# Kernel optimization log

Hardware: AMD Instinct MI355X
Metric: run time of the kernel (lower is better)

## Reference

```python
import jax, jax.numpy as jnp
import numpy as np

N, D_MODEL, D_FFN, K = 8192, 1024, 4096, 512


def setup_inputs() -> dict:
    key = jax.random.key(0)
    ks = jax.random.split(key, 5)
    x = jax.random.normal(ks[0], (N, D_MODEL), dtype=jnp.float32)
    topk_indices = jax.random.randint(ks[1], (N, K), 0, D_FFN, dtype=jnp.int32)
    scale = 0.02
    w_gate = jax.random.normal(ks[2], (D_MODEL, D_FFN), dtype=jnp.float32) * scale
    w_up = jax.random.normal(ks[3], (D_MODEL, D_FFN), dtype=jnp.float32) * scale
    w_down = jax.random.normal(ks[4], (D_FFN, D_MODEL), dtype=jnp.float32) * scale
    return {"x": x, "topk_indices": topk_indices, "w_gate": w_gate, "w_up": w_up, "w_down": w_down}


def reference(x, topk_indices, w_gate, w_up, w_down):
    # Dense gate/up projections: [N, d_ffn]
    G = x @ w_gate
    U = x @ w_up
    # Gather only the top-k active neurons per token and fuse SwiGLU there.
    G_act = jnp.take_along_axis(G, topk_indices, axis=1)  # [N, k]
    U_act = jnp.take_along_axis(U, topk_indices, axis=1)  # [N, k]
    Z_active = jax.nn.silu(G_act) * U_act                 # [N, k]
    # Sparse-to-dense down projection: scatter active activations back into
    # the d_ffn axis (zeros elsewhere), then dense matmul with w_down.
    n, k = topk_indices.shape
    rows = jnp.arange(n, dtype=topk_indices.dtype)[:, None]
    Z_dense = jnp.zeros((n, w_down.shape[0]), dtype=Z_active.dtype).at[rows, topk_indices].add(Z_active)
    return Z_dense @ w_down  # [N, d_model]
```

## Files before the change

### kernel.cpp

```cpp
#include <hip/hip_runtime.h>
#include <hip/hip_bf16.h>
#include <cstdint>
#include <cstddef>

#define N_TOK   8192
#define D_MODEL 1024
#define D_FFN   4096
#define K_TOP   512
#define NHALF   2048

typedef __bf16 bf16_t;
typedef __bf16 bf16x8 __attribute__((ext_vector_type(8)));
typedef __bf16 bf16x4 __attribute__((ext_vector_type(4)));
typedef float  f32x4  __attribute__((ext_vector_type(4)));


__global__ void cvt_f32_bf16(const float* __restrict__ in, bf16_t* __restrict__ out, int n4) {
  int i = blockIdx.x * blockDim.x + threadIdx.x;
  if (i < n4) {
    const f32x4 v = ((const f32x4*)in)[i];
    bf16x4 o;
    o[0] = (bf16_t)v[0]; o[1] = (bf16_t)v[1]; o[2] = (bf16_t)v[2]; o[3] = (bf16_t)v[3];
    ((bf16x4*)out)[i] = o;
  }
}

__global__ void transpose_cvt(const float* __restrict__ in, bf16_t* __restrict__ out,
                              int rows, int cols) {
  __shared__ float tile[32][33];
  const int tx = threadIdx.x, ty = threadIdx.y;
  const int x = blockIdx.x * 32 + tx;
#pragma unroll
  for (int i = 0; i < 32; i += 8) {
    int y = blockIdx.y * 32 + ty + i;
    tile[ty + i][tx] = in[(size_t)y * cols + x];
  }
  __syncthreads();
  const int xo = blockIdx.y * 32 + tx;
#pragma unroll
  for (int i = 0; i < 32; i += 8) {
    int yo = blockIdx.x * 32 + ty + i;
    out[(size_t)yo * rows + xo] = (bf16_t)tile[tx][ty + i];
  }
}

#define ROWS_PER_BLK 4
__global__ __launch_bounds__(256) void count_scatter_lds(
    const int* __restrict__ idx, unsigned int* __restrict__ M) {
  __shared__ unsigned int loc[ROWS_PER_BLK * (D_FFN / 8)];
  const int t = threadIdx.x;
  const int r0 = blockIdx.x * ROWS_PER_BLK;

#pragma unroll
  for (int i = 0; i < ROWS_PER_BLK * (D_FFN / 8) / 256; ++i)
    loc[t + i * 256] = 0;
  __syncthreads();

  const int* ip = idx + (size_t)r0 * K_TOP;
#pragma unroll
  for (int i = 0; i < ROWS_PER_BLK * K_TOP / 256; ++i) {
    const int e = t + i * 256;
    const int lr = e >> 9;
    const int j = ip[e];
    atomicAdd(&loc[lr * (D_FFN / 8) + (j >> 3)], 1u << ((j & 7) * 4));
  }
  __syncthreads();

  unsigned int* op = M + (size_t)r0 * (D_FFN / 8);
#pragma unroll
  for (int i = 0; i < ROWS_PER_BLK * (D_FFN / 8) / 256; ++i)
    op[t + i * 256] = loc[t + i * 256];
}


__device__ __forceinline__ void gload_lds16(const void* g, void* l) {
#if __has_builtin(__builtin_amdgcn_global_load_lds)
  __builtin_amdgcn_global_load_lds((__attribute__((address_space(1))) void*)(g),
                                   (__attribute__((address_space(3))) void*)(l), 16, 0, 0);
#else
  *(bf16x8*)l = *(const bf16x8*)g;
#endif
}

#define MFMA16(ACC, AF, BF)                                                      \
  _Pragma("unroll")                                                              \
  for (int m = 0; m < 4; ++m)                                                    \
    _Pragma("unroll")                                                            \
    for (int n = 0; n < 4; ++n)                                                  \
      ACC[m][n] = __builtin_amdgcn_mfma_f32_16x16x32_bf16(AF[m], BF[n], ACC[m][n], 0, 0, 0);

#define BM1 256
#define BN1 128
#define BK1 64
#define NT1 (D_MODEL / BK1)
#define LDSBUF 65536

__global__ __launch_bounds__(512, 2) void gemm_gateup_2p(
    const bf16_t* __restrict__ A,
    const bf16_t* __restrict__ Bg,
    const bf16_t* __restrict__ Bu,
    const unsigned int* __restrict__ cnt,
    bf16_t* __restrict__ Z,
    int n_base)
{
  extern __shared__ char smem[];
  const int t = threadIdx.x;
  const int lane = t & 63;
  const int w = t >> 6;
  const int wr = w >> 1;
  const int wc = w & 1;
  const int l15 = lane & 15;
  const int grp = lane >> 4;
  const int m0 = blockIdx.x * BM1;
  const int n0 = blockIdx.y * BN1;

  int offA[4], offB[2];
#pragma unroll
  for (int c = 0; c < 4; ++c) {
    const int s = c * 512 + w * 64 + lane;
    const int r = s >> 3, cb = (s & 7) ^ (r & 7);
    offA[c] = (m0 + r) * D_MODEL + cb * 8;
  }
#pragma unroll
  for (int c = 0; c < 2; ++c) {
    const int s = c * 512 + w * 64 + lane;
    const int r = s >> 3, cb = (s & 7) ^ (r & 7);
    offB[c] = (n_base + n0 + r) * D_MODEL + cb * 8;
  }
  const int dst0 = (w * 64 + lane) * 16;

  const int swz = l15 & 7;
  const int a_k0 = wr * 8192 + l15 * 128 + ((0 + grp) ^ swz) * 16;
  const int a_k1 = wr * 8192 + l15 * 128 + ((4 + grp) ^ swz) * 16;
  const int bg_k0 = 32768 + wc * 8192 + l15 * 128 + ((0 + grp) ^ swz) * 16;
  const int bg_k1 = 32768 + wc * 8192 + l15 * 128 + ((4 + grp) ^ swz) * 16;
  const int bu_k0 = bg_k0 + 16384;
  const int bu_k1 = bg_k1 + 16384;

#pragma unroll
  for (int c = 0; c < 4; ++c) gload_lds16(A + offA[c], smem + dst0 + c * 8192);
#pragma unroll
  for (int c = 0; c < 2; ++c) gload_lds16(Bg + offB[c], smem + 32768 + dst0 + c * 8192);
#pragma unroll
  for (int c = 0; c < 2; ++c) gload_lds16(Bu + offB[c], smem + 49152 + dst0 + c * 8192);
  asm volatile("s_waitcnt vmcnt(0)" ::: "memory");
  __builtin_amdgcn_s_barrier();

  f32x4 accg[4][4] = {};
  f32x4 accu[4][4] = {};

  for (int tt = 0; tt < NT1; ++tt) {
    char* rb = smem + (tt & 1) * LDSBUF;
    char* wb = smem + ((tt & 1) ^ 1) * LDSBUF;
    const int kg = (tt + 1) * BK1;
    const bool st = (tt + 1 < NT1);
    bf16x8 af0[4], af1[4], bg0[4], bg1[4], bu0[4], bu1[4];

#pragma unroll
    for (int m = 0; m < 4; ++m) {
      af0[m] = *(const bf16x8*)(rb + a_k0 + m * 2048);
      af1[m] = *(const bf16x8*)(rb + a_k1 + m * 2048);
    }
#pragma unroll
    for (int n = 0; n < 4; ++n) {
      bg0[n] = *(const bf16x8*)(rb + bg_k0 + n * 2048);
      bg1[n] = *(const bf16x8*)(rb + bg_k1 + n * 2048);
    }
    if (st) {
#pragma unroll
      for (int c = 0; c < 4; ++c) gload_lds16(A + offA[c] + kg, wb + dst0 + c * 8192);
#pragma unroll
      for (int c = 0; c < 2; ++c) gload_lds16(Bg + offB[c] + kg, wb + 32768 + dst0 + c * 8192);
#pragma unroll
      for (int c = 0; c < 2; ++c) gload_lds16(Bu + offB[c] + kg, wb + 49152 + dst0 + c * 8192);
    }
    __builtin_amdgcn_s_barrier();
    asm volatile("s_waitcnt lgkmcnt(0)" ::: "memory");
    __builtin_amdgcn_s_setprio(1);
    MFMA16(accg, af0, bg0);
    MFMA16(accg, af1, bg1);
    __builtin_amdgcn_s_setprio(0);
    __builtin_amdgcn_s_barrier();

#pragma unroll
    for (int n = 0; n < 4; ++n) {
      bu0[n] = *(const bf16x8*)(rb + bu_k0 + n * 2048);
      bu1[n] = *(const bf16x8*)(rb + bu_k1 + n * 2048);
    }
    asm volatile("s_waitcnt lgkmcnt(0)" ::: "memory");
    __builtin_amdgcn_s_setprio(1);
    MFMA16(accu, af0, bu0);
    MFMA16(accu, af1, bu1);
    __builtin_amdgcn_s_setprio(0);
    if (st) asm volatile("s_waitcnt vmcnt(0)" ::: "memory");
    __builtin_amdgcn_s_barrier();
  }

#pragma unroll
  for (int m = 0; m < 4; ++m) {
#pragma unroll
    for (int n = 0; n < 4; ++n) {
      const int colL = n0 + wc * 64 + n * 16 + l15;
      const int jg = n_base + colL;
#pragma unroll
      for (int j = 0; j < 4; ++j) {
        const int row = m0 + wr * 64 + m * 16 + grp * 4 + j;
        float g = accg[m][n][j];
        float u = accu[m][n][j];
        unsigned int cw = cnt[(size_t)row * (D_FFN / 8) + (jg >> 3)];
        float c = (float)((cw >> ((jg & 7) * 4)) & 15u);
        float z = c * u * (g / (1.0f + __expf(-g)));
        Z[(size_t)row * NHALF + colL] = (bf16_t)z;
      }
    }
  }
}

#define BM2 256
#define BN2 128
#define BK2 64
#define NT2 (NHALF / BK2)
#define LDSBUF2 49152

__global__ __launch_bounds__(512, 2) void gemm_down_1p(
    const bf16_t* __restrict__ A,
    const bf16_t* __restrict__ B,
    float* __restrict__ C,
    int k_base, int accum)
{
  extern __shared__ char smem[];
  const int t = threadIdx.x;
  const int lane = t & 63;
  const int w = t >> 6;
  const int wr = w >> 1;
  const int wc = w & 1;
  const int l15 = lane & 15;
  const int grp = lane >> 4;
  const int m0 = blockIdx.x * BM2;
  const int n0 = blockIdx.y * BN2;

  int offA[4], offB[2];
#pragma unroll
  for (int c = 0; c < 4; ++c) {
    const int s = c * 512 + w * 64 + lane;
    const int r = s >> 3, cb = (s & 7) ^ (r & 7);
    offA[c] = (m0 + r) * NHALF + cb * 8;
  }
#pragma unroll
  for (int c = 0; c < 2; ++c) {
    const int s = c * 512 + w * 64 + lane;
    const int r = s >> 3, cb = (s & 7) ^ (r & 7);
    offB[c] = (n0 + r) * D_FFN + k_base + cb * 8;
  }
  const int dst0 = (w * 64 + lane) * 16;

  const int swz = l15 & 7;
  const int a_k0 = wr * 8192 + l15 * 128 + ((0 + grp) ^ swz) * 16;
  const int a_k1 = wr * 8192 + l15 * 128 + ((4 + grp) ^ swz) * 16;
  const int b_k0 = 32768 + wc * 8192 + l15 * 128 + ((0 + grp) ^ swz) * 16;
  const int b_k1 = 32768 + wc * 8192 + l15 * 128 + ((4 + grp) ^ swz) * 16;

#pragma unroll
  for (int c = 0; c < 4; ++c) gload_lds16(A + offA[c], smem + dst0 + c * 8192);
#pragma unroll
  for (int c = 0; c < 2; ++c) gload_lds16(B + offB[c], smem + 32768 + dst0 + c * 8192);
  asm volatile("s_waitcnt vmcnt(0)" ::: "memory");
  __builtin_amdgcn_s_barrier();

  f32x4 acc[4][4] = {};

  for (int tt = 0; tt < NT2; ++tt) {
    char* rb = smem + (tt & 1) * LDSBUF2;
    char* wb = smem + ((tt & 1) ^ 1) * LDSBUF2;
    const int kg = (tt + 1) * BK2;
    const bool st = (tt + 1 < NT2);
    bf16x8 af0[4], af1[4], bf0[4], bf1[4];

#pragma unroll
    for (int m = 0; m < 4; ++m) {
      af0[m] = *(const bf16x8*)(rb + a_k0 + m * 2048);
      af1[m] = *(const bf16x8*)(rb + a_k1 + m * 2048);
    }
#pragma unroll
    for (int n = 0; n < 4; ++n) {
      bf0[n] = *(const bf16x8*)(rb + b_k0 + n * 2048);
      bf1[n] = *(const bf16x8*)(rb + b_k1 + n * 2048);
    }
    if (st) {
#pragma unroll
      for (int c = 0; c < 4; ++c) gload_lds16(A + offA[c] + kg, wb + dst0 + c * 8192);
#pragma unroll
      for (int c = 0; c < 2; ++c) gload_lds16(B + offB[c] + kg, wb + 32768 + dst0 + c * 8192);
    }
    __builtin_amdgcn_s_barrier();
    asm volatile("s_waitcnt lgkmcnt(0)" ::: "memory");
    __builtin_amdgcn_s_setprio(1);
    MFMA16(acc, af0, bf0);
    MFMA16(acc, af1, bf1);
    __builtin_amdgcn_s_setprio(0);
    if (st) asm volatile("s_waitcnt vmcnt(0)" ::: "memory");
    __builtin_amdgcn_s_barrier();
  }

#pragma unroll
  for (int m = 0; m < 4; ++m) {
#pragma unroll
    for (int n = 0; n < 4; ++n) {
      const int col = n0 + wc * 64 + n * 16 + l15;
#pragma unroll
      for (int j = 0; j < 4; ++j) {
        const int row = m0 + wr * 64 + m * 16 + grp * 4 + j;
        const size_t off = (size_t)row * D_MODEL + col;
        float prev = accum ? C[off] : 0.0f;
        C[off] = prev + acc[m][n][j];
      }
    }
  }
}


extern "C" void kernel_launch(void* const* d_in, const int* in_sizes, int n_in,
                              void* d_out, int out_size, void* d_ws, size_t ws_size,
                              hipStream_t stream) {
  const float* x  = (const float*)d_in[0];
  const int*   idx = (const int*)d_in[1];
  const float* wg = (const float*)d_in[2];
  const float* wu = (const float*)d_in[3];
  const float* wd = (const float*)d_in[4];
  float* out = (float*)d_out;

  char* ws = (char*)d_ws;
  const size_t SZ_XB  = (size_t)N_TOK * D_MODEL * 2;
  const size_t SZ_W   = (size_t)D_MODEL * D_FFN * 2;
  const size_t SZ_CNT = (size_t)N_TOK * D_FFN / 2;
  bf16_t* xb  = (bf16_t*)(ws);
  bf16_t* wgT = (bf16_t*)(ws + SZ_XB);
  bf16_t* wuT = (bf16_t*)(ws + SZ_XB + SZ_W);
  bf16_t* wdT = (bf16_t*)(ws + SZ_XB + 2 * SZ_W);
  unsigned int* cnt = (unsigned int*)(ws + SZ_XB + 3 * SZ_W);
  bf16_t* Z   = (bf16_t*)(ws + SZ_XB + 3 * SZ_W + SZ_CNT);

  (void)hipFuncSetAttribute((const void*)gemm_gateup_2p,
                            hipFuncAttributeMaxDynamicSharedMemorySize, 131072);
  (void)hipFuncSetAttribute((const void*)gemm_down_1p,
                            hipFuncAttributeMaxDynamicSharedMemorySize, 98304);

  count_scatter_lds<<<N_TOK / ROWS_PER_BLK, 256, 0, stream>>>(idx, cnt);
  cvt_f32_bf16<<<(N_TOK * D_MODEL / 4 + 255) / 256, 256, 0, stream>>>(x, xb, N_TOK * D_MODEL / 4);
  transpose_cvt<<<dim3(D_FFN / 32, D_MODEL / 32), dim3(32, 8), 0, stream>>>(wg, wgT, D_MODEL, D_FFN);
  transpose_cvt<<<dim3(D_FFN / 32, D_MODEL / 32), dim3(32, 8), 0, stream>>>(wu, wuT, D_MODEL, D_FFN);
  transpose_cvt<<<dim3(D_MODEL / 32, D_FFN / 32), dim3(32, 8), 0, stream>>>(wd, wdT, D_FFN, D_MODEL);

  gemm_gateup_2p<<<dim3(N_TOK / BM1, NHALF / BN1), 512, 131072, stream>>>(xb, wgT, wuT, cnt, Z, 0);
  gemm_down_1p<<<dim3(N_TOK / BM2, D_MODEL / BN2), 512, 98304, stream>>>(Z, wdT, out, 0, 0);
  gemm_gateup_2p<<<dim3(N_TOK / BM1, NHALF / BN1), 512, 131072, stream>>>(xb, wgT, wuT, cnt, Z, NHALF);
  gemm_down_1p<<<dim3(N_TOK / BM2, D_MODEL / BN2), 512, 98304, stream>>>(Z, wdT, out, NHALF, 1);
}
```

Baseline: 266.5 us.

## Switch gate/up and down GEMMs to triple-buffered BK=32 pipelines with register prefetch

Both GEMM kernels move from double-buffered BK=64 tiles to triple-buffered BK=32 tiles. Global-to-LDS loads are issued two stages ahead, and the next tile's LDS fragments are prefetched into registers during the MFMAs, which leaves one barrier per iteration instead of two. LDS use drops to 96KB and 72KB, and the down kernel's launch bounds ask for 4 blocks per CU. The goal is to hide memory latency and cut barrier stalls, at the cost of more iterations, tighter vmcnt bookkeeping and possible register pressure.

```diff
diff --git a/kernel.cpp b/kernel.cpp
--- a/kernel.cpp
+++ b/kernel.cpp
@@ -89,13 +89,14 @@
     for (int n = 0; n < 4; ++n)                                                  \
       ACC[m][n] = __builtin_amdgcn_mfma_f32_16x16x32_bf16(AF[m], BF[n], ACC[m][n], 0, 0, 0);
 
+
 #define BM1 256
 #define BN1 128
-#define BK1 64
+#define BK1 32
 #define NT1 (D_MODEL / BK1)
-#define LDSBUF 65536
-
-__global__ __launch_bounds__(512, 2) void gemm_gateup_2p(
+#define GU_BUF 32768
+
+__global__ __launch_bounds__(512, 2) void gemm_gateup_3b(
     const bf16_t* __restrict__ A,
     const bf16_t* __restrict__ Bg,
     const bf16_t* __restrict__ Bu,
@@ -114,86 +115,72 @@
   const int m0 = blockIdx.x * BM1;
   const int n0 = blockIdx.y * BN1;
 
-  int offA[4], offB[2];
-#pragma unroll
-  for (int c = 0; c < 4; ++c) {
-    const int s = c * 512 + w * 64 + lane;
-    const int r = s >> 3, cb = (s & 7) ^ (r & 7);
-    offA[c] = (m0 + r) * D_MODEL + cb * 8;
-  }
-#pragma unroll
-  for (int c = 0; c < 2; ++c) {
-    const int s = c * 512 + w * 64 + lane;
-    const int r = s >> 3, cb = (s & 7) ^ (r & 7);
-    offB[c] = (n_base + n0 + r) * D_MODEL + cb * 8;
-  }
-  const int dst0 = (w * 64 + lane) * 16;
-
-  const int swz = l15 & 7;
-  const int a_k0 = wr * 8192 + l15 * 128 + ((0 + grp) ^ swz) * 16;
-  const int a_k1 = wr * 8192 + l15 * 128 + ((4 + grp) ^ swz) * 16;
-  const int bg_k0 = 32768 + wc * 8192 + l15 * 128 + ((0 + grp) ^ swz) * 16;
-  const int bg_k1 = 32768 + wc * 8192 + l15 * 128 + ((4 + grp) ^ swz) * 16;
-  const int bu_k0 = bg_k0 + 16384;
-  const int bu_k1 = bg_k1 + 16384;
-
-#pragma unroll
-  for (int c = 0; c < 4; ++c) gload_lds16(A + offA[c], smem + dst0 + c * 8192);
-#pragma unroll
-  for (int c = 0; c < 2; ++c) gload_lds16(Bg + offB[c], smem + 32768 + dst0 + c * 8192);
-#pragma unroll
-  for (int c = 0; c < 2; ++c) gload_lds16(Bu + offB[c], smem + 49152 + dst0 + c * 8192);
-  asm volatile("s_waitcnt vmcnt(0)" ::: "memory");
+  const int sA0 = t, sA1 = t + 512;
+  const int rA0 = sA0 >> 2, uA0 = (sA0 & 3) ^ (rA0 & 3);
+  const int rA1 = sA1 >> 2, uA1 = (sA1 & 3) ^ (rA1 & 3);
+  const int rB  = t >> 2,   uB  = (t & 3) ^ (rB & 3);
+  const int gA0 = (m0 + rA0) * D_MODEL + uA0 * 8;
+  const int gA1 = (m0 + rA1) * D_MODEL + uA1 * 8;
+  const int gB  = (n_base + n0 + rB) * D_MODEL + uB * 8;
+  const int dA0 = sA0 * 16, dA1 = sA1 * 16, dB = t * 16;
+
+#define GU_STAGE(ti) do {                                                        \
+    char* _b = smem + ((ti) % 3) * GU_BUF; const int _k = (ti) * BK1;            \
+    gload_lds16(A  + gA0 + _k, _b + dA0);                                        \
+    gload_lds16(A  + gA1 + _k, _b + dA1);                                        \
+    gload_lds16(Bg + gB  + _k, _b + 16384 + dB);                                 \
+    gload_lds16(Bu + gB  + _k, _b + 24576 + dB); } while (0)
+
+  int a_off[4], bg_off[4];
+#pragma unroll
+  for (int m = 0; m < 4; ++m) {
+    const int row = wr * 64 + m * 16 + l15;
+    a_off[m] = row * 64 + ((grp ^ (row & 3)) * 16);
+  }
+#pragma unroll
+  for (int n = 0; n < 4; ++n) {
+    const int row = wc * 64 + n * 16 + l15;
+    bg_off[n] = 16384 + row * 64 + ((grp ^ (row & 3)) * 16);
+  }
+
+  GU_STAGE(0); GU_STAGE(1);
+  asm volatile("s_waitcnt vmcnt(4)" ::: "memory");
   __builtin_amdgcn_s_barrier();
+
+  bf16x8 af[4], bgf[4], buf_[4];
+#pragma unroll
+  for (int m = 0; m < 4; ++m) af[m] = *(const bf16x8*)(smem + a_off[m]);
+#pragma unroll
+  for (int n = 0; n < 4; ++n) bgf[n] = *(const bf16x8*)(smem + bg_off[n]);
 
   f32x4 accg[4][4] = {};
   f32x4 accu[4][4] = {};
 
   for (int tt = 0; tt < NT1; ++tt) {
-    char* rb = smem + (tt & 1) * LDSBUF;
-    char* wb = smem + ((tt & 1) ^ 1) * LDSBUF;
-    const int kg = (tt + 1) * BK1;
-    const bool st = (tt + 1 < NT1);
-    bf16x8 af0[4], af1[4], bg0[4], bg1[4], bu0[4], bu1[4];
-
-#pragma unroll
-    for (int m = 0; m < 4; ++m) {
-      af0[m] = *(const bf16x8*)(rb + a_k0 + m * 2048);
-      af1[m] = *(const bf16x8*)(rb + a_k1 + m * 2048);
-    }
-#pragma unroll
-    for (int n = 0; n < 4; ++n) {
-      bg0[n] = *(const bf16x8*)(rb + bg_k0 + n * 2048);
-      bg1[n] = *(const bf16x8*)(rb + bg_k1 + n * 2048);
-    }
-    if (st) {
-#pragma unroll
-      for (int c = 0; c < 4; ++c) gload_lds16(A + offA[c] + kg, wb + dst0 + c * 8192);
-#pragma unroll
-      for (int c = 0; c < 2; ++c) gload_lds16(Bg + offB[c] + kg, wb + 32768 + dst0 + c * 8192);
-#pragma unroll
-      for (int c = 0; c < 2; ++c) gload_lds16(Bu + offB[c] + kg, wb + 49152 + dst0 + c * 8192);
-    }
+    char* rbuf = smem + (tt % 3) * GU_BUF;
+    if (tt + 2 < NT1) GU_STAGE(tt + 2);
+#pragma unroll
+    for (int n = 0; n < 4; ++n) buf_[n] = *(const bf16x8*)(rbuf + bg_off[n] + 8192);
+    asm volatile("s_waitcnt lgkmcnt(4)" ::: "memory");
+    __builtin_amdgcn_s_setprio(1);
+    MFMA16(accg, af, bgf);
+    __builtin_amdgcn_s_setprio(0);
+    asm volatile("s_waitcnt lgkmcnt(0)" ::: "memory");
+    if (tt + 2 < NT1) { asm volatile("s_waitcnt vmcnt(4)" ::: "memory"); }
+    else              { asm volatile("s_waitcnt vmcnt(0)" ::: "memory"); }
     __builtin_amdgcn_s_barrier();
-    asm volatile("s_waitcnt lgkmcnt(0)" ::: "memory");
+    char* nbuf = smem + ((tt + 1) % 3) * GU_BUF;
+    if (tt + 1 < NT1) {
+#pragma unroll
+      for (int n = 0; n < 4; ++n) bgf[n] = *(const bf16x8*)(nbuf + bg_off[n]);
+    }
     __builtin_amdgcn_s_setprio(1);
-    MFMA16(accg, af0, bg0);
-    MFMA16(accg, af1, bg1);
+    MFMA16(accu, af, buf_);
     __builtin_amdgcn_s_setprio(0);
-    __builtin_amdgcn_s_barrier();
-
-#pragma unroll
-    for (int n = 0; n < 4; ++n) {
-      bu0[n] = *(const bf16x8*)(rb + bu_k0 + n * 2048);
-      bu1[n] = *(const bf16x8*)(rb + bu_k1 + n * 2048);
-    }
-    asm volatile("s_waitcnt lgkmcnt(0)" ::: "memory");
-    __builtin_amdgcn_s_setprio(1);
-    MFMA16(accu, af0, bu0);
-    MFMA16(accu, af1, bu1);
-    __builtin_amdgcn_s_setprio(0);
-    if (st) asm volatile("s_waitcnt vmcnt(0)" ::: "memory");
-    __builtin_amdgcn_s_barrier();
+    if (tt + 1 < NT1) {
+#pragma unroll
+      for (int m = 0; m < 4; ++m) af[m] = *(const bf16x8*)(nbuf + a_off[m]);
+    }
   }
 
 #pragma unroll
@@ -214,16 +201,17 @@
       }
     }
   }
+#undef GU_STAGE
 }
 
 #define BM2 256
 #define BN2 128
-#define BK2 64
+#define BK2 32
 #define NT2 (NHALF / BK2)
-#define LDSBUF2 49152
-
-__global__ __launch_bounds__(512, 2) void gemm_down_1p(
-    const bf16_t* __restrict__ A,
+#define DN_BUF 24576
+
+__global__ __launch_bounds__(512, 4) void gemm_down_3b(
+    const bf16_t* __restrict__ Az,
     const bf16_t* __restrict__ B,
     float* __restrict__ C,
     int k_base, int accum)
@@ -239,67 +227,61 @@
   const int m0 = blockIdx.x * BM2;
   const int n0 = blockIdx.y * BN2;
 
-  int offA[4], offB[2];
-#pragma unroll
-  for (int c = 0; c < 4; ++c) {
-    const int s = c * 512 + w * 64 + lane;
-    const int r = s >> 3, cb = (s & 7) ^ (r & 7);
-    offA[c] = (m0 + r) * NHALF + cb * 8;
-  }
-#pragma unroll
-  for (int c = 0; c < 2; ++c) {
-    const int s = c * 512 + w * 64 + lane;
-    const int r = s >> 3, cb = (s & 7) ^ (r & 7);
-    offB[c] = (n0 + r) * D_FFN + k_base + cb * 8;
-  }
-  const int dst0 = (w * 64 + lane) * 16;
-
-  const int swz = l15 & 7;
-  const int a_k0 = wr * 8192 + l15 * 128 + ((0 + grp) ^ swz) * 16;
-  const int a_k1 = wr * 8192 + l15 * 128 + ((4 + grp) ^ swz) * 16;
-  const int b_k0 = 32768 + wc * 8192 + l15 * 128 + ((0 + grp) ^ swz) * 16;
-  const int b_k1 = 32768 + wc * 8192 + l15 * 128 + ((4 + grp) ^ swz) * 16;
-
-#pragma unroll
-  for (int c = 0; c < 4; ++c) gload_lds16(A + offA[c], smem + dst0 + c * 8192);
-#pragma unroll
-  for (int c = 0; c < 2; ++c) gload_lds16(B + offB[c], smem + 32768 + dst0 + c * 8192);
-  asm volatile("s_waitcnt vmcnt(0)" ::: "memory");
+  const int sA0 = t, sA1 = t + 512;
+  const int rA0 = sA0 >> 2, uA0 = (sA0 & 3) ^ (rA0 & 3);
+  const int rA1 = sA1 >> 2, uA1 = (sA1 & 3) ^ (rA1 & 3);
+  const int rB  = t >> 2,   uB  = (t & 3) ^ (rB & 3);
+  const int gA0 = (m0 + rA0) * NHALF + uA0 * 8;
+  const int gA1 = (m0 + rA1) * NHALF + uA1 * 8;
+  const int gB  = (n0 + rB) * D_FFN + k_base + uB * 8;
+  const int dA0 = sA0 * 16, dA1 = sA1 * 16, dB = t * 16;
+
+#define DN_STAGE(ti) do {                                                        \
+    char* _b = smem + ((ti) % 3) * DN_BUF; const int _k = (ti) * BK2;            \
+    gload_lds16(Az + gA0 + _k, _b + dA0);                                        \
+    gload_lds16(Az + gA1 + _k, _b + dA1);                                        \
+    gload_lds16(B  + gB  + _k, _b + 16384 + dB); } while (0)
+
+  int a_off[4], b_off[4];
+#pragma unroll
+  for (int m = 0; m < 4; ++m) {
+    const int row = wr * 64 + m * 16 + l15;
+    a_off[m] = row * 64 + ((grp ^ (row & 3)) * 16);
+  }
+#pragma unroll
+  for (int n = 0; n < 4; ++n) {
+    const int row = wc * 64 + n * 16 + l15;
+    b_off[n] = 16384 + row * 64 + ((grp ^ (row & 3)) * 16);
+  }
+
+  DN_STAGE(0); DN_STAGE(1);
+  asm volatile("s_waitcnt vmcnt(3)" ::: "memory");
   __builtin_amdgcn_s_barrier();
 
+  bf16x8 af[4], bf[4];
+#pragma unroll
+  for (int m = 0; m < 4; ++m) af[m] = *(const bf16x8*)(smem + a_off[m]);
+#pragma unroll
+  for (int n = 0; n < 4; ++n) bf[n] = *(const bf16x8*)(smem + b_off[n]);
+
   f32x4 acc[4][4] = {};
 
   for (int tt = 0; tt < NT2; ++tt) {
-    char* rb = smem + (tt & 1) * LDSBUF2;
-    char* wb = smem + ((tt & 1) ^ 1) * LDSBUF2;
-    const int kg = (tt + 1) * BK2;
-    const bool st = (tt + 1 < NT2);
-    bf16x8 af0[4], af1[4], bf0[4], bf1[4];
-
-#pragma unroll
-    for (int m = 0; m < 4; ++m) {
-      af0[m] = *(const bf16x8*)(rb + a_k0 + m * 2048);
-      af1[m] = *(const bf16x8*)(rb + a_k1 + m * 2048);
-    }
-#pragma unroll
-    for (int n = 0; n < 4; ++n) {
-      bf0[n] = *(const bf16x8*)(rb + b_k0 + n * 2048);
-      bf1[n] = *(const bf16x8*)(rb + b_k1 + n * 2048);
-    }
-    if (st) {
-#pragma unroll
-      for (int c = 0; c < 4; ++c) gload_lds16(A + offA[c] + kg, wb + dst0 + c * 8192);
-#pragma unroll
-      for (int c = 0; c < 2; ++c) gload_lds16(B + offB[c] + kg, wb + 32768 + dst0 + c * 8192);
-    }
+    if (tt + 2 < NT2) DN_STAGE(tt + 2);
+    __builtin_amdgcn_s_setprio(1);
+    MFMA16(acc, af, bf);
+    __builtin_amdgcn_s_setprio(0);
+    asm volatile("s_waitcnt lgkmcnt(0)" ::: "memory");
+    if (tt + 2 < NT2) { asm volatile("s_waitcnt vmcnt(3)" ::: "memory"); }
+    else              { asm volatile("s_waitcnt vmcnt(0)" ::: "memory"); }
     __builtin_amdgcn_s_barrier();
-    asm volatile("s_waitcnt lgkmcnt(0)" ::: "memory");
-    __builtin_amdgcn_s_setprio(1);
-    MFMA16(acc, af0, bf0);
-    MFMA16(acc, af1, bf1);
-    __builtin_amdgcn_s_setprio(0);
-    if (st) asm volatile("s_waitcnt vmcnt(0)" ::: "memory");
-    __builtin_amdgcn_s_barrier();
+    if (tt + 1 < NT2) {
+      char* nbuf = smem + ((tt + 1) % 3) * DN_BUF;
+#pragma unroll
+      for (int m = 0; m < 4; ++m) af[m] = *(const bf16x8*)(nbuf + a_off[m]);
+#pragma unroll
+      for (int n = 0; n < 4; ++n) bf[n] = *(const bf16x8*)(nbuf + b_off[n]);
+    }
   }
 
 #pragma unroll
@@ -316,6 +298,7 @@
       }
     }
   }
+#undef DN_STAGE
 }
 
 
@@ -340,10 +323,10 @@
   unsigned int* cnt = (unsigned int*)(ws + SZ_XB + 3 * SZ_W);
   bf16_t* Z   = (bf16_t*)(ws + SZ_XB + 3 * SZ_W + SZ_CNT);
 
-  (void)hipFuncSetAttribute((const void*)gemm_gateup_2p,
-                            hipFuncAttributeMaxDynamicSharedMemorySize, 131072);
-  (void)hipFuncSetAttribute((const void*)gemm_down_1p,
-                            hipFuncAttributeMaxDynamicSharedMemorySize, 98304);
+  (void)hipFuncSetAttribute((const void*)gemm_gateup_3b,
+                            hipFuncAttributeMaxDynamicSharedMemorySize, 3 * GU_BUF);
+  (void)hipFuncSetAttribute((const void*)gemm_down_3b,
+                            hipFuncAttributeMaxDynamicSharedMemorySize, 3 * DN_BUF);
 
   count_scatter_lds<<<N_TOK / ROWS_PER_BLK, 256, 0, stream>>>(idx, cnt);
   cvt_f32_bf16<<<(N_TOK * D_MODEL / 4 + 255) / 256, 256, 0, stream>>>(x, xb, N_TOK * D_MODEL / 4);
@@ -351,8 +334,8 @@
   transpose_cvt<<<dim3(D_FFN / 32, D_MODEL / 32), dim3(32, 8), 0, stream>>>(wu, wuT, D_MODEL, D_FFN);
   transpose_cvt<<<dim3(D_MODEL / 32, D_FFN / 32), dim3(32, 8), 0, stream>>>(wd, wdT, D_FFN, D_MODEL);
 
-  gemm_gateup_2p<<<dim3(N_TOK / BM1, NHALF / BN1), 512, 131072, stream>>>(xb, wgT, wuT, cnt, Z, 0);
-  gemm_down_1p<<<dim3(N_TOK / BM2, D_MODEL / BN2), 512, 98304, stream>>>(Z, wdT, out, 0, 0);
-  gemm_gateup_2p<<<dim3(N_TOK / BM1, NHALF / BN1), 512, 131072, stream>>>(xb, wgT, wuT, cnt, Z, NHALF);
-  gemm_down_1p<<<dim3(N_TOK / BM2, D_MODEL / BN2), 512, 98304, stream>>>(Z, wdT, out, NHALF, 1);
-}
+  gemm_gateup_3b<<<dim3(N_TOK / BM1, NHALF / BN1), 512, 3 * GU_BUF, stream>>>(xb, wgT, wuT, cnt, Z, 0);
+  gemm_down_3b<<<dim3(N_TOK / BM2, D_MODEL / BN2), 512, 3 * DN_BUF, stream>>>(Z, wdT, out, 0, 0);
+  gemm_gateup_3b<<<dim3(N_TOK / BM1, NHALF / BN1), 512, 3 * GU_BUF, stream>>>(xb, wgT, wuT, cnt, Z, NHALF);
+  gemm_down_3b<<<dim3(N_TOK / BM2, D_MODEL / BN2), 512, 3 * DN_BUF, stream>>>(Z, wdT, out, NHALF, 1);
+}
```

New measurement: 271.1 us. About the same (+1.7%).
